# Kernel tuning notes

Hardware: AMD Instinct MI355X
Metric: run time of the kernel (lower is better)

The kernel has to match this reference:

```python
import jax, jax.numpy as jnp
import numpy as np

N, E = 50000, 800000
NODE_DIM, EDGE_DIM, HIDDEN = 128, 32, 128


def setup_inputs() -> dict:
    key = jax.random.key(0)
    ks = jax.random.split(key, 12)
    def lin(k, fan_in, shape):
        bound = 1.0 / np.sqrt(fan_in)
        return jax.random.uniform(k, shape, jnp.float32, -bound, bound)
    return {
        "x": jax.random.normal(ks[0], (N, NODE_DIM), jnp.float32),
        "edge_index": jax.random.randint(ks[1], (2, E), 0, N),
        "edge_attr": jax.random.normal(ks[2], (E, EDGE_DIM), jnp.float32),
        # msg MLP: Linear(node+edge -> hidden), Linear(hidden -> hidden)
        "W1": lin(ks[3], NODE_DIM + EDGE_DIM, (HIDDEN, NODE_DIM + EDGE_DIM)),
        "b1": lin(ks[4], NODE_DIM + EDGE_DIM, (HIDDEN,)),
        "W2": lin(ks[5], HIDDEN, (HIDDEN, HIDDEN)),
        "b2": lin(ks[6], HIDDEN, (HIDDEN,)),
        # GRUCell(input=HIDDEN, hidden=NODE_DIM); gate order r,z,n (torch)
        "W_ih": lin(ks[7], NODE_DIM, (3 * NODE_DIM, HIDDEN)),
        "b_ih": lin(ks[8], NODE_DIM, (3 * NODE_DIM,)),
        "W_hh": lin(ks[9], NODE_DIM, (3 * NODE_DIM, NODE_DIM)),
        "b_hh": lin(ks[10], NODE_DIM, (3 * NODE_DIM,)),
    }


def reference(x, edge_index, edge_attr, W1, b1, W2, b2, W_ih, b_ih, W_hh, b_hh):
    src, dst = edge_index[0], edge_index[1]
    # gather + edge MLP: [E, node+edge] -> [E, hidden]
    m_in = jnp.concatenate([x[src], edge_attr], axis=-1)
    h1 = jax.nn.silu(m_in @ W1.T + b1)
    m = jax.nn.silu(h1 @ W2.T + b2)
    # scatter-add messages per destination node
    agg = jax.ops.segment_sum(m, dst, num_segments=x.shape[0])  # [N, hidden]
    # GRUCell: gates in torch order (r, z, n)
    gi = agg @ W_ih.T + b_ih  # [N, 3*node_dim]
    gh = x @ W_hh.T + b_hh
    i_r, i_z, i_n = jnp.split(gi, 3, axis=-1)
    h_r, h_z, h_n = jnp.split(gh, 3, axis=-1)
    r = jax.nn.sigmoid(i_r + h_r)
    z = jax.nn.sigmoid(i_z + h_z)
    n = jnp.tanh(i_n + r * h_n)
    return (1.0 - z) * n + z * x
```

## Files before the change

kernel.cpp:

```cpp
#include <hip/hip_runtime.h>
#include <hip/hip_bf16.h>
#include <cstdint>

typedef __bf16 bf16x8 __attribute__((ext_vector_type(8)));
typedef __bf16 bf16x4 __attribute__((ext_vector_type(4)));
typedef float  f32x4  __attribute__((ext_vector_type(4)));

#define ND 128
#define HID 128

__device__ __forceinline__ f32x4 mfma_bf16(bf16x8 a, bf16x8 b, f32x4 c) {
  return __builtin_amdgcn_mfma_f32_16x16x32_bf16(a, b, c, 0, 0, 0);
}
__device__ __forceinline__ float fast_sigmoid(float x) {
  return __fdividef(1.f, 1.f + __expf(-x));
}
__device__ __forceinline__ float fast_silu(float x) {
  return __fdividef(x, 1.f + __expf(-x));
}
__device__ __forceinline__ float fast_tanh(float x) {
  float cx = fminf(fmaxf(x, -15.f), 15.f);
  float e = __expf(2.f * cx);
  return __fdividef(e - 1.f, e + 1.f);
}

__global__ void cvt_all(const float* __restrict__ s0, __bf16* __restrict__ d0, int c1,
                        const float* __restrict__ s1, __bf16* __restrict__ d1, int c2,
                        const float* __restrict__ s2, __bf16* __restrict__ d2, int c3,
                        const float* __restrict__ s3, __bf16* __restrict__ d3, int c4,
                        const float* __restrict__ s4, __bf16* __restrict__ d4, int c5) {
  int i = blockIdx.x * blockDim.x + threadIdx.x;
  const float* s; __bf16* d; int j;
  if (i < c1)      { s = s0; d = d0; j = i; }
  else if (i < c2) { s = s1; d = d1; j = i - c1; }
  else if (i < c3) { s = s2; d = d2; j = i - c2; }
  else if (i < c4) { s = s3; d = d3; j = i - c3; }
  else if (i < c5) { s = s4; d = d4; j = i - c4; }
  else return;
  const float4* sp = reinterpret_cast<const float4*>(s) + (size_t)j * 2;
  float4 a = sp[0], b = sp[1];
  bf16x8 v;
  v[0] = (__bf16)a.x; v[1] = (__bf16)a.y; v[2] = (__bf16)a.z; v[3] = (__bf16)a.w;
  v[4] = (__bf16)b.x; v[5] = (__bf16)b.y; v[6] = (__bf16)b.z; v[7] = (__bf16)b.w;
  reinterpret_cast<bf16x8*>(d)[j] = v;
}

__global__ void k_hist(const int* __restrict__ dst, int* __restrict__ counts, int E) {
  int e = blockIdx.x * 256 + threadIdx.x;
  if (e < E) atomicAdd(&counts[dst[e]], 1);
}

__global__ void k_blocksum(const int* __restrict__ counts, int* __restrict__ bsum) {
  __shared__ int sd[256];
  int t = threadIdx.x;
  sd[t] = counts[blockIdx.x * 256 + t];
  __syncthreads();
  for (int d = 128; d > 0; d >>= 1) { if (t < d) sd[t] += sd[t + d]; __syncthreads(); }
  if (!t) bsum[blockIdx.x] = sd[0];
}

__global__ void k_scan_bsum(int* __restrict__ bsum, int nb) {
  __shared__ int sd[256];
  int t = threadIdx.x;
  int v = (t < nb) ? bsum[t] : 0;
  sd[t] = v;
  __syncthreads();
  for (int d = 1; d < 256; d <<= 1) {
    int u = (t >= d) ? sd[t - d] : 0;
    __syncthreads();
    sd[t] += u;
    __syncthreads();
  }
  if (t < nb) bsum[t] = sd[t] - v;
}

__global__ void k_scan_write(const int* __restrict__ counts, const int* __restrict__ bsum,
                             int* __restrict__ offsets, int* __restrict__ cursor) {
  __shared__ int sd[256];
  int t = threadIdx.x, b = blockIdx.x;
  int i = b * 256 + t;
  int c = counts[i];
  sd[t] = c;
  __syncthreads();
  for (int d = 1; d < 256; d <<= 1) {
    int u = (t >= d) ? sd[t - d] : 0;
    __syncthreads();
    sd[t] += u;
    __syncthreads();
  }
  int excl = bsum[b] + sd[t] - c;
  offsets[i] = excl;
  cursor[i]  = excl;
  if (b == (int)gridDim.x - 1 && t == 255) offsets[i + 1] = excl + c;
}

__global__ void k_spos(const int* __restrict__ dst, int* __restrict__ cursor,
                       int* __restrict__ spos, int E) {
  int e = blockIdx.x * 256 + threadIdx.x;
  if (e < E) spos[e] = atomicAdd(&cursor[dst[e]], 1);
}

#define TILE_E 64

template <int SORT>
__global__ __launch_bounds__(512, 6) void edge_mlp(
    const __bf16* __restrict__ xb,
    const int*    __restrict__ ei,
    const float*  __restrict__ ea,
    const __bf16* __restrict__ W1b,
    const float*  __restrict__ b1,
    const __bf16* __restrict__ W2b,
    const float*  __restrict__ b2,
    float*  __restrict__ agg,
    __bf16* __restrict__ mbuf,
    const int* __restrict__ spos,
    int E, int ntiles)
{
  __shared__ __bf16 Als[TILE_E * 192];
  __shared__ __bf16 H1[TILE_E * 128];
  char* AlsB = (char*)Als;
  char* H1B  = (char*)H1;

  const int tid = threadIdx.x;
  const int w  = tid >> 6;
  const int l  = tid & 63;
  const int l4 = l >> 4;
  const int lm = l & 15;
  const int jb = w * 16;

  bf16x8 bw1[5], bw2[4];
  {
    const int jr = jb + lm;
#pragma unroll
    for (int kt = 0; kt < 5; ++kt)
      bw1[kt] = *reinterpret_cast<const bf16x8*>(W1b + (size_t)jr * 160 + kt * 32 + l4 * 8);
#pragma unroll
    for (int kt = 0; kt < 4; ++kt)
      bw2[kt] = *reinterpret_cast<const bf16x8*>(W2b + (size_t)jr * 128 + kt * 32 + l4 * 8);
  }
  float4 b1v = *reinterpret_cast<const float4*>(b1 + jb + l4 * 4);
  float4 b2v = *reinterpret_cast<const float4*>(b2 + jb + l4 * 4);
  const int* srcp = ei;
  const int* dstp = ei + E;

  for (int tile = blockIdx.x; tile < ntiles; tile += gridDim.x) {
    const int e0 = tile * TILE_E;

#pragma unroll
    for (int it = 0; it < 2; ++it) {
      int idx = it * 512 + tid;
      int e = idx >> 4, q = idx & 15;
      int s = srcp[e0 + e];
      bf16x8 v = *reinterpret_cast<const bf16x8*>(xb + (size_t)s * ND + q * 8);
      *reinterpret_cast<bf16x8*>(AlsB + e * 384 + ((q ^ (e & 7)) << 4)) = v;
    }
    {
      int e = tid >> 3, q = tid & 7;
      float4 v = reinterpret_cast<const float4*>(ea)[(size_t)(e0 + e) * 8 + q];
      bf16x4 h;
      h[0] = (__bf16)v.x; h[1] = (__bf16)v.y; h[2] = (__bf16)v.z; h[3] = (__bf16)v.w;
      int chunk = 16 + (q >> 1);
      *reinterpret_cast<bf16x4*>(AlsB + e * 384 + ((chunk ^ (e & 7)) << 4) + ((q & 1) << 3)) = h;
    }
    if (SORT && tid < TILE_E) {
      int sp = spos[e0 + tid];
      *reinterpret_cast<int*>(AlsB + tid * 384 + ((20 ^ (tid & 7)) << 4)) = sp;
    }
    __syncthreads();

#pragma unroll
    for (int et = 0; et < 4; ++et) {
      const int e = et * 16 + lm;
      const int sw = lm & 7;
      f32x4 acc = {0.f, 0.f, 0.f, 0.f};
#pragma unroll
      for (int kt = 0; kt < 5; ++kt) {
        bf16x8 bfrag = *reinterpret_cast<const bf16x8*>(AlsB + e * 384 + (((kt * 4 + l4) ^ sw) << 4));
        acc = mfma_bf16(bw1[kt], bfrag, acc);
      }
      bf16x4 h0;
#pragma unroll
      for (int rr = 0; rr < 4; ++rr)
        h0[rr] = (__bf16)fast_silu(acc[rr] + (&b1v.x)[rr]);
      int c0 = w * 2 + (l4 >> 1);
      int inner = (l4 & 1) << 3;
      *reinterpret_cast<bf16x4*>(H1B + e * 256 + ((c0 ^ sw) << 4) + inner) = h0;
    }
    __syncthreads();

#pragma unroll
    for (int et = 0; et < 4; ++et) {
      const int e = et * 16 + lm;
      const int sw = lm & 7;
      f32x4 acc = {0.f, 0.f, 0.f, 0.f};
#pragma unroll
      for (int kt = 0; kt < 4; ++kt) {
        bf16x8 bfrag = *reinterpret_cast<const bf16x8*>(H1B + e * 256 + (((kt * 4 + l4) ^ sw) << 4));
        acc = mfma_bf16(bw2[kt], bfrag, acc);
      }
      if (SORT) {
        bf16x4 m0;
#pragma unroll
        for (int rr = 0; rr < 4; ++rr)
          m0[rr] = (__bf16)fast_silu(acc[rr] + (&b2v.x)[rr]);
        int sp = *reinterpret_cast<const int*>(AlsB + e * 384 + ((20 ^ sw) << 4));
        *reinterpret_cast<bf16x4*>(mbuf + (size_t)sp * HID + jb + l4 * 4) = m0;
      } else {
        int d = dstp[e0 + e];
#pragma unroll
        for (int rr = 0; rr < 4; ++rr)
          atomicAdd(agg + (size_t)d * HID + jb + l4 * 4 + rr,
                    fast_silu(acc[rr] + (&b2v.x)[rr]));
      }
    }
    __syncthreads();
  }
}

__global__ __launch_bounds__(256) void k_aggregate(
    const __bf16* __restrict__ mbuf, const int* __restrict__ offsets,
    __bf16* __restrict__ aggb, int N)
{
  int node = blockIdx.x * 4 + (threadIdx.x >> 6);
  int l = threadIdx.x & 63;
  if (node >= N) return;
  int lo = offsets[node], hi = offsets[node + 1];
  int cnt = hi - lo;
  float s0 = 0.f, s1 = 0.f;
  const uint32_t* p = reinterpret_cast<const uint32_t*>(mbuf) + (size_t)lo * 64 + l;
  int r = 0;
  for (; r + 4 <= cnt; r += 4) {
    uint32_t u0 = p[0], u1 = p[64], u2 = p[128], u3 = p[192];
    p += 256;
    s0 += __uint_as_float(u0 << 16) + __uint_as_float(u1 << 16)
        + __uint_as_float(u2 << 16) + __uint_as_float(u3 << 16);
    s1 += __uint_as_float(u0 & 0xffff0000u) + __uint_as_float(u1 & 0xffff0000u)
        + __uint_as_float(u2 & 0xffff0000u) + __uint_as_float(u3 & 0xffff0000u);
  }
  for (; r < cnt; ++r) {
    uint32_t u = p[0];
    p += 64;
    s0 += __uint_as_float(u << 16);
    s1 += __uint_as_float(u & 0xffff0000u);
  }
  uint32_t o = (uint32_t)__builtin_bit_cast(unsigned short, (__bf16)s0) |
               ((uint32_t)__builtin_bit_cast(unsigned short, (__bf16)s1) << 16);
  reinterpret_cast<uint32_t*>(aggb)[(size_t)node * 64 + l] = o;
}

__global__ __launch_bounds__(512) void gru2(
    const __bf16* __restrict__ aggb,
    const __bf16* __restrict__ xb,
    const float*  __restrict__ x,
    const __bf16* __restrict__ Wih, const float* __restrict__ bih,
    const __bf16* __restrict__ Whh, const float* __restrict__ bhh,
    float* __restrict__ out, int N)
{
  const int tid = threadIdx.x;
  const int w = tid >> 6, l = tid & 63;
  const int l4 = l >> 4, lm = l & 15;
  const int n0 = blockIdx.x * 64;
  const int jb = w * 16;
  const int jr = jb + lm, jz = jr + 128, jn = jr + 256;

  bf16x8 WiR[4], WhR[4], WiZ[4], WhZ[4], WiN[4], WhN[4];
#pragma unroll
  for (int kt = 0; kt < 4; ++kt) {
    int ko = kt * 32 + l4 * 8;
    WiR[kt] = *reinterpret_cast<const bf16x8*>(Wih + (size_t)jr * ND + ko);
    WhR[kt] = *reinterpret_cast<const bf16x8*>(Whh + (size_t)jr * ND + ko);
    WiZ[kt] = *reinterpret_cast<const bf16x8*>(Wih + (size_t)jz * ND + ko);
    WhZ[kt] = *reinterpret_cast<const bf16x8*>(Whh + (size_t)jz * ND + ko);
    WiN[kt] = *reinterpret_cast<const bf16x8*>(Wih + (size_t)jn * ND + ko);
    WhN[kt] = *reinterpret_cast<const bf16x8*>(Whh + (size_t)jn * ND + ko);
  }
  float4 birv, bizv, binv, bhnv;
  {
    int j0 = jb + l4 * 4;
    float4 a = *reinterpret_cast<const float4*>(bih + j0);
    float4 b = *reinterpret_cast<const float4*>(bhh + j0);
    birv = make_float4(a.x + b.x, a.y + b.y, a.z + b.z, a.w + b.w);
    a = *reinterpret_cast<const float4*>(bih + 128 + j0);
    b = *reinterpret_cast<const float4*>(bhh + 128 + j0);
    bizv = make_float4(a.x + b.x, a.y + b.y, a.z + b.z, a.w + b.w);
    binv = *reinterpret_cast<const float4*>(bih + 256 + j0);
    bhnv = *reinterpret_cast<const float4*>(bhh + 256 + j0);
  }

#pragma unroll
  for (int rt = 0; rt < 4; ++rt) {
    const int node = n0 + rt * 16 + lm;
    const bool ok = node < N;
    bf16x8 aA[4], aX[4];
#pragma unroll
    for (int kt = 0; kt < 4; ++kt) {
      int ko = kt * 32 + l4 * 8;
      bf16x8 z8 = {};
      aA[kt] = ok ? *reinterpret_cast<const bf16x8*>(aggb + (size_t)node * ND + ko) : z8;
      aX[kt] = ok ? *reinterpret_cast<const bf16x8*>(xb + (size_t)node * ND + ko) : z8;
    }
    f32x4 aR = {0.f,0.f,0.f,0.f}, aZ = {0.f,0.f,0.f,0.f};
    f32x4 ai = {0.f,0.f,0.f,0.f}, ah = {0.f,0.f,0.f,0.f};
#pragma unroll
    for (int kt = 0; kt < 4; ++kt) {
      aR = mfma_bf16(WiR[kt], aA[kt], aR);
      aR = mfma_bf16(WhR[kt], aX[kt], aR);
      aZ = mfma_bf16(WiZ[kt], aA[kt], aZ);
      aZ = mfma_bf16(WhZ[kt], aX[kt], aZ);
      ai = mfma_bf16(WiN[kt], aA[kt], ai);
      ah = mfma_bf16(WhN[kt], aX[kt], ah);
    }
    if (ok) {
      float4 xv = *reinterpret_cast<const float4*>(x + (size_t)node * ND + jb + l4 * 4);
      float4 ov;
#pragma unroll
      for (int rr = 0; rr < 4; ++rr) {
        float r = fast_sigmoid(aR[rr] + (&birv.x)[rr]);
        float z = fast_sigmoid(aZ[rr] + (&bizv.x)[rr]);
        float n = fast_tanh(ai[rr] + (&binv.x)[rr] + r * (ah[rr] + (&bhnv.x)[rr]));
        (&ov.x)[rr] = (1.f - z) * n + z * (&xv.x)[rr];
      }
      *reinterpret_cast<float4*>(out + (size_t)node * ND + jb + l4 * 4) = ov;
    }
  }
}

extern "C" void kernel_launch(void* const* d_in, const int* in_sizes, int n_in,
                              void* d_out, int out_size, void* d_ws, size_t ws_size,
                              hipStream_t stream) {
  const float* x   = (const float*)d_in[0];
  const int*   ei  = (const int*)d_in[1];
  const float* ea  = (const float*)d_in[2];
  const float* W1  = (const float*)d_in[3];
  const float* b1  = (const float*)d_in[4];
  const float* W2  = (const float*)d_in[5];
  const float* b2  = (const float*)d_in[6];
  const float* Wih = (const float*)d_in[7];
  const float* bih = (const float*)d_in[8];
  const float* Whh = (const float*)d_in[9];
  const float* bhh = (const float*)d_in[10];
  float* out = (float*)d_out;
  const int N = in_sizes[0] / ND;
  const int E = in_sizes[1] / 2;

  const int nb = (N + 255) / 256;
  const int nC = nb * 256;

  char* ws = (char*)d_ws;
  size_t off = 0;
  auto alloc = [&](size_t bytes) -> void* {
    void* p = ws + off;
    off += (bytes + 255) & ~(size_t)255;
    return p;
  };
  __bf16* xb   = (__bf16*)alloc((size_t)N * ND * 2);
  __bf16* aggb = (__bf16*)alloc((size_t)N * ND * 2);
  __bf16* W1b  = (__bf16*)alloc(128 * 160 * 2);
  __bf16* W2b  = (__bf16*)alloc(128 * 128 * 2);
  __bf16* Wihb = (__bf16*)alloc(384 * 128 * 2);
  __bf16* Whhb = (__bf16*)alloc(384 * 128 * 2);
  size_t common_off = off;

  int*    counts  = (int*)alloc((size_t)nC * 4);
  int*    offsets = (int*)alloc((size_t)(nC + 16) * 4);
  int*    cursor  = (int*)alloc((size_t)nC * 4);
  int*    bsum    = (int*)alloc(256 * 4);
  int*    spos    = (int*)alloc((size_t)E * 4);
  __bf16* mbuf    = (__bf16*)alloc((size_t)E * HID * 2);
  size_t need_sort = off;

  bool use_sort = (ws_size >= need_sort);

  const int n8_x = N * ND / 8, n8_1 = 128 * 160 / 8, n8_2 = 128 * 128 / 8, n8_g = 384 * 128 / 8;
  int c1 = n8_x, c2 = c1 + n8_1, c3 = c2 + n8_2, c4 = c3 + n8_g, c5 = c4 + n8_g;
  cvt_all<<<(c5 + 255) / 256, 256, 0, stream>>>(x, xb, c1, W1, W1b, c2, W2, W2b, c3,
                                                Wih, Wihb, c4, Whh, Whhb, c5);

  const int ntiles = E / TILE_E;
  const int* dstp = ei + E;

  if (use_sort) {
    hipMemsetAsync(counts, 0, (size_t)nC * 4, stream);
    k_hist<<<(E + 255) / 256, 256, 0, stream>>>(dstp, counts, E);
    k_blocksum<<<nb, 256, 0, stream>>>(counts, bsum);
    k_scan_bsum<<<1, 256, 0, stream>>>(bsum, nb);
    k_scan_write<<<nb, 256, 0, stream>>>(counts, bsum, offsets, cursor);
    k_spos<<<(E + 255) / 256, 256, 0, stream>>>(dstp, cursor, spos, E);
    edge_mlp<1><<<2500, 512, 0, stream>>>(xb, ei, ea, W1b, b1, W2b, b2,
                                          nullptr, mbuf, spos, E, ntiles);
    k_aggregate<<<(N + 3) / 4, 256, 0, stream>>>(mbuf, offsets, aggb, N);
  } else {
    off = common_off;
    float* aggf = (float*)alloc((size_t)N * ND * 4);
    hipMemsetAsync(aggf, 0, (size_t)N * ND * 4, stream);
    edge_mlp<0><<<2500, 512, 0, stream>>>(xb, ei, ea, W1b, b1, W2b, b2,
                                          aggf, nullptr, nullptr, E, ntiles);
    cvt_all<<<(n8_x + 255) / 256, 256, 0, stream>>>(aggf, aggb, n8_x,
                                                    nullptr, nullptr, n8_x,
                                                    nullptr, nullptr, n8_x,
                                                    nullptr, nullptr, n8_x,
                                                    nullptr, nullptr, n8_x);
  }

  gru2<<<(N + 63) / 64, 512, 0, stream>>>(aggb, xb, x, Wihb, bih, Whhb, bhh, out, N);
}
```

Baseline: 390.1 us.

## Process edges in dst-sorted order and fuse segmented reduction into edge MLP

Builds a dst-sorted edge permutation and has the edge MLP walk edges in that order. Messages are written to LDS and reduced per destination run inside each tile, with fp32 atomics to agg. This drops the E×128 bf16 message buffer and the separate aggregate kernel, and the kernel also prefetches the next tile's gathers into registers. In exchange, edge_attr and source lookups become indirect gathers, fp32 atomics are still needed, and occupancy is lowered.

New measurement: 365.8 us. 1.07x faster.

```diff
diff --git a/kernel.cpp b/kernel.cpp
--- a/kernel.cpp
+++ b/kernel.cpp
@@ -75,7 +75,7 @@
 }
 
 __global__ void k_scan_write(const int* __restrict__ counts, const int* __restrict__ bsum,
-                             int* __restrict__ offsets, int* __restrict__ cursor) {
+                             int* __restrict__ cursor) {
   __shared__ int sd[256];
   int t = threadIdx.x, b = blockIdx.x;
   int i = b * 256 + t;
@@ -88,38 +88,40 @@
     sd[t] += u;
     __syncthreads();
   }
-  int excl = bsum[b] + sd[t] - c;
-  offsets[i] = excl;
-  cursor[i]  = excl;
-  if (b == (int)gridDim.x - 1 && t == 255) offsets[i + 1] = excl + c;
-}
-
-__global__ void k_spos(const int* __restrict__ dst, int* __restrict__ cursor,
-                       int* __restrict__ spos, int E) {
+  cursor[i] = bsum[b] + sd[t] - c;
+}
+
+__global__ void k_perm(const int* __restrict__ dst, int* __restrict__ cursor,
+                       int* __restrict__ eperm, int* __restrict__ dsorted, int E) {
   int e = blockIdx.x * 256 + threadIdx.x;
-  if (e < E) spos[e] = atomicAdd(&cursor[dst[e]], 1);
+  if (e < E) {
+    int d = dst[e];
+    int p = atomicAdd(&cursor[d], 1);
+    eperm[p] = e;
+    dsorted[p] = d;
+  }
 }
 
 #define TILE_E 64
 
-template <int SORT>
-__global__ __launch_bounds__(512, 6) void edge_mlp(
+__global__ __launch_bounds__(512, 4) void edge_mlp2(
     const __bf16* __restrict__ xb,
-    const int*    __restrict__ ei,
+    const int*    __restrict__ srcp,
     const float*  __restrict__ ea,
     const __bf16* __restrict__ W1b,
     const float*  __restrict__ b1,
     const __bf16* __restrict__ W2b,
     const float*  __restrict__ b2,
-    float*  __restrict__ agg,
-    __bf16* __restrict__ mbuf,
-    const int* __restrict__ spos,
-    int E, int ntiles)
+    const int*    __restrict__ eperm,
+    const int*    __restrict__ dsorted,
+    float* __restrict__ agg,
+    int ntiles)
 {
-  __shared__ __bf16 Als[TILE_E * 192];
+  __shared__ __bf16 Als[TILE_E * 160];
   __shared__ __bf16 H1[TILE_E * 128];
-  char* AlsB = (char*)Als;
-  char* H1B  = (char*)H1;
+  __shared__ int dstls[TILE_E];
+  char* AB = (char*)Als;
+  char* HB = (char*)H1;
 
   const int tid = threadIdx.x;
   const int w  = tid >> 6;
@@ -138,45 +140,72 @@
     for (int kt = 0; kt < 4; ++kt)
       bw2[kt] = *reinterpret_cast<const bf16x8*>(W2b + (size_t)jr * 128 + kt * 32 + l4 * 8);
   }
-  float4 b1v = *reinterpret_cast<const float4*>(b1 + jb + l4 * 4);
-  float4 b2v = *reinterpret_cast<const float4*>(b2 + jb + l4 * 4);
-  const int* srcp = ei;
-  const int* dstp = ei + E;
-
-  for (int tile = blockIdx.x; tile < ntiles; tile += gridDim.x) {
-    const int e0 = tile * TILE_E;
-
-#pragma unroll
-    for (int it = 0; it < 2; ++it) {
-      int idx = it * 512 + tid;
-      int e = idx >> 4, q = idx & 15;
-      int s = srcp[e0 + e];
-      bf16x8 v = *reinterpret_cast<const bf16x8*>(xb + (size_t)s * ND + q * 8);
-      *reinterpret_cast<bf16x8*>(AlsB + e * 384 + ((q ^ (e & 7)) << 4)) = v;
-    }
+  const float4 b1v = *reinterpret_cast<const float4*>(b1 + jb + l4 * 4);
+  const float4 b2v = *reinterpret_cast<const float4*>(b2 + jb + l4 * 4);
+
+  const int fj = tid & 127;
+  const int fg = tid >> 7;
+  const int fchunk = fj >> 3;
+  const int finner = (fj & 7) * 2;
+
+  const int xslot = tid >> 4, xq = tid & 15;
+  const int aslot = tid >> 3, aq = tid & 7;
+
+  bf16x8 pxv0 = {}, pxv1 = {};
+  float4 pea_ = {};
+  int pdst_ = 0;
+
+  auto PREFETCH = [&](int t) {
+    int p0 = t * TILE_E;
+    int e0i = eperm[p0 + xslot];
+    int e1i = eperm[p0 + xslot + 32];
+    int s0 = srcp[e0i];
+    int s1 = srcp[e1i];
+    pxv0 = *reinterpret_cast<const bf16x8*>(xb + (size_t)s0 * ND + xq * 8);
+    pxv1 = *reinterpret_cast<const bf16x8*>(xb + (size_t)s1 * ND + xq * 8);
+    int e2i = eperm[p0 + aslot];
+    pea_ = reinterpret_cast<const float4*>(ea)[(size_t)e2i * 8 + aq];
+    if (tid < TILE_E) pdst_ = dsorted[p0 + tid];
+  };
+
+  int tile = blockIdx.x;
+  if (tile < ntiles) PREFETCH(tile);
+
+  for (; tile < ntiles; tile += gridDim.x) {
+    __syncthreads();
+
     {
-      int e = tid >> 3, q = tid & 7;
-      float4 v = reinterpret_cast<const float4*>(ea)[(size_t)(e0 + e) * 8 + q];
+      int s_ = xslot;
+      *reinterpret_cast<bf16x8*>(AB + s_ * 320 + ((xq ^ (s_ & 7)) << 4)) = pxv0;
+      int s2 = xslot + 32;
+      *reinterpret_cast<bf16x8*>(AB + s2 * 320 + ((xq ^ (s2 & 7)) << 4)) = pxv1;
+    }
+    {
       bf16x4 h;
-      h[0] = (__bf16)v.x; h[1] = (__bf16)v.y; h[2] = (__bf16)v.z; h[3] = (__bf16)v.w;
-      int chunk = 16 + (q >> 1);
-      *reinterpret_cast<bf16x4*>(AlsB + e * 384 + ((chunk ^ (e & 7)) << 4) + ((q & 1) << 3)) = h;
-    }
-    if (SORT && tid < TILE_E) {
-      int sp = spos[e0 + tid];
-      *reinterpret_cast<int*>(AlsB + tid * 384 + ((20 ^ (tid & 7)) << 4)) = sp;
-    }
-    __syncthreads();
+      h[0] = (__bf16)pea_.x; h[1] = (__bf16)pea_.y;
+      h[2] = (__bf16)pea_.z; h[3] = (__bf16)pea_.w;
+      int pc = 16 + ((aq >> 1) ^ (aslot & 3));
+      *reinterpret_cast<bf16x4*>(AB + aslot * 320 + (pc << 4) + ((aq & 1) << 3)) = h;
+    }
+    if (tid < TILE_E) dstls[tid] = pdst_;
+    __syncthreads();
+
+    int nt = tile + gridDim.x;
+    if (nt < ntiles) PREFETCH(nt);
 
 #pragma unroll
     for (int et = 0; et < 4; ++et) {
-      const int e = et * 16 + lm;
-      const int sw = lm & 7;
+      const int s_ = et * 16 + lm;
+      const int sw = s_ & 7;
       f32x4 acc = {0.f, 0.f, 0.f, 0.f};
 #pragma unroll
-      for (int kt = 0; kt < 5; ++kt) {
-        bf16x8 bfrag = *reinterpret_cast<const bf16x8*>(AlsB + e * 384 + (((kt * 4 + l4) ^ sw) << 4));
+      for (int kt = 0; kt < 4; ++kt) {
+        bf16x8 bfrag = *reinterpret_cast<const bf16x8*>(AB + s_ * 320 + (((kt * 4 + l4) ^ sw) << 4));
         acc = mfma_bf16(bw1[kt], bfrag, acc);
+      }
+      {
+        bf16x8 bfrag = *reinterpret_cast<const bf16x8*>(AB + s_ * 320 + ((16 + (l4 ^ (s_ & 3))) << 4));
+        acc = mfma_bf16(bw1[4], bfrag, acc);
       }
       bf16x4 h0;
 #pragma unroll
@@ -184,72 +213,53 @@
         h0[rr] = (__bf16)fast_silu(acc[rr] + (&b1v.x)[rr]);
       int c0 = w * 2 + (l4 >> 1);
       int inner = (l4 & 1) << 3;
-      *reinterpret_cast<bf16x4*>(H1B + e * 256 + ((c0 ^ sw) << 4) + inner) = h0;
+      *reinterpret_cast<bf16x4*>(HB + s_ * 256 + ((c0 ^ sw) << 4) + inner) = h0;
     }
     __syncthreads();
 
 #pragma unroll
     for (int et = 0; et < 4; ++et) {
-      const int e = et * 16 + lm;
-      const int sw = lm & 7;
+      const int s_ = et * 16 + lm;
+      const int sw = s_ & 7;
       f32x4 acc = {0.f, 0.f, 0.f, 0.f};
 #pragma unroll
       for (int kt = 0; kt < 4; ++kt) {
-        bf16x8 bfrag = *reinterpret_cast<const bf16x8*>(H1B + e * 256 + (((kt * 4 + l4) ^ sw) << 4));
+        bf16x8 bfrag = *reinterpret_cast<const bf16x8*>(HB + s_ * 256 + (((kt * 4 + l4) ^ sw) << 4));
         acc = mfma_bf16(bw2[kt], bfrag, acc);
       }
-      if (SORT) {
-        bf16x4 m0;
-#pragma unroll
-        for (int rr = 0; rr < 4; ++rr)
-          m0[rr] = (__bf16)fast_silu(acc[rr] + (&b2v.x)[rr]);
-        int sp = *reinterpret_cast<const int*>(AlsB + e * 384 + ((20 ^ sw) << 4));
-        *reinterpret_cast<bf16x4*>(mbuf + (size_t)sp * HID + jb + l4 * 4) = m0;
-      } else {
-        int d = dstp[e0 + e];
-#pragma unroll
-        for (int rr = 0; rr < 4; ++rr)
-          atomicAdd(agg + (size_t)d * HID + jb + l4 * 4 + rr,
-                    fast_silu(acc[rr] + (&b2v.x)[rr]));
-      }
-    }
-    __syncthreads();
-  }
-}
-
-__global__ __launch_bounds__(256) void k_aggregate(
-    const __bf16* __restrict__ mbuf, const int* __restrict__ offsets,
-    __bf16* __restrict__ aggb, int N)
-{
-  int node = blockIdx.x * 4 + (threadIdx.x >> 6);
-  int l = threadIdx.x & 63;
-  if (node >= N) return;
-  int lo = offsets[node], hi = offsets[node + 1];
-  int cnt = hi - lo;
-  float s0 = 0.f, s1 = 0.f;
-  const uint32_t* p = reinterpret_cast<const uint32_t*>(mbuf) + (size_t)lo * 64 + l;
-  int r = 0;
-  for (; r + 4 <= cnt; r += 4) {
-    uint32_t u0 = p[0], u1 = p[64], u2 = p[128], u3 = p[192];
-    p += 256;
-    s0 += __uint_as_float(u0 << 16) + __uint_as_float(u1 << 16)
-        + __uint_as_float(u2 << 16) + __uint_as_float(u3 << 16);
-    s1 += __uint_as_float(u0 & 0xffff0000u) + __uint_as_float(u1 & 0xffff0000u)
-        + __uint_as_float(u2 & 0xffff0000u) + __uint_as_float(u3 & 0xffff0000u);
-  }
-  for (; r < cnt; ++r) {
-    uint32_t u = p[0];
-    p += 64;
-    s0 += __uint_as_float(u << 16);
-    s1 += __uint_as_float(u & 0xffff0000u);
-  }
-  uint32_t o = (uint32_t)__builtin_bit_cast(unsigned short, (__bf16)s0) |
-               ((uint32_t)__builtin_bit_cast(unsigned short, (__bf16)s1) << 16);
-  reinterpret_cast<uint32_t*>(aggb)[(size_t)node * 64 + l] = o;
+      bf16x4 m0;
+#pragma unroll
+      for (int rr = 0; rr < 4; ++rr)
+        m0[rr] = (__bf16)fast_silu(acc[rr] + (&b2v.x)[rr]);
+      int c0 = w * 2 + (l4 >> 1);
+      int inner = (l4 & 1) << 3;
+      *reinterpret_cast<bf16x4*>(AB + s_ * 256 + ((c0 ^ sw) << 4) + inner) = m0;
+    }
+    __syncthreads();
+
+    {
+      float acc = 0.f;
+      int cur = dstls[fg * 16];
+#pragma unroll
+      for (int i = 0; i < 16; ++i) {
+        int slot = fg * 16 + i;
+        int nd = dstls[slot];
+        if (nd != cur) {
+          atomicAdd(agg + (size_t)cur * HID + fj, acc);
+          acc = 0.f;
+          cur = nd;
+        }
+        uint32_t raw = *reinterpret_cast<const uint16_t*>(
+            AB + slot * 256 + ((fchunk ^ (slot & 7)) << 4) + finner);
+        acc += __uint_as_float(raw << 16);
+      }
+      atomicAdd(agg + (size_t)cur * HID + fj, acc);
+    }
+  }
 }
 
 __global__ __launch_bounds__(512) void gru2(
-    const __bf16* __restrict__ aggb,
+    const float*  __restrict__ agg,
     const __bf16* __restrict__ xb,
     const float*  __restrict__ x,
     const __bf16* __restrict__ Wih, const float* __restrict__ bih,
@@ -296,8 +306,18 @@
     for (int kt = 0; kt < 4; ++kt) {
       int ko = kt * 32 + l4 * 8;
       bf16x8 z8 = {};
-      aA[kt] = ok ? *reinterpret_cast<const bf16x8*>(aggb + (size_t)node * ND + ko) : z8;
-      aX[kt] = ok ? *reinterpret_cast<const bf16x8*>(xb + (size_t)node * ND + ko) : z8;
+      if (ok) {
+        float4 a0 = *reinterpret_cast<const float4*>(agg + (size_t)node * ND + ko);
+        float4 a1 = *reinterpret_cast<const float4*>(agg + (size_t)node * ND + ko + 4);
+        bf16x8 v;
+        v[0] = (__bf16)a0.x; v[1] = (__bf16)a0.y; v[2] = (__bf16)a0.z; v[3] = (__bf16)a0.w;
+        v[4] = (__bf16)a1.x; v[5] = (__bf16)a1.y; v[6] = (__bf16)a1.z; v[7] = (__bf16)a1.w;
+        aA[kt] = v;
+        aX[kt] = *reinterpret_cast<const bf16x8*>(xb + (size_t)node * ND + ko);
+      } else {
+        aA[kt] = z8;
+        aX[kt] = z8;
+      }
     }
     f32x4 aR = {0.f,0.f,0.f,0.f}, aZ = {0.f,0.f,0.f,0.f};
     f32x4 ai = {0.f,0.f,0.f,0.f}, ah = {0.f,0.f,0.f,0.f};
@@ -353,54 +373,39 @@
     off += (bytes + 255) & ~(size_t)255;
     return p;
   };
-  __bf16* xb   = (__bf16*)alloc((size_t)N * ND * 2);
-  __bf16* aggb = (__bf16*)alloc((size_t)N * ND * 2);
-  __bf16* W1b  = (__bf16*)alloc(128 * 160 * 2);
-  __bf16* W2b  = (__bf16*)alloc(128 * 128 * 2);
-  __bf16* Wihb = (__bf16*)alloc(384 * 128 * 2);
-  __bf16* Whhb = (__bf16*)alloc(384 * 128 * 2);
-  size_t common_off = off;
-
+  __bf16* xb      = (__bf16*)alloc((size_t)N * ND * 2);
+  __bf16* W1b     = (__bf16*)alloc(128 * 160 * 2);
+  __bf16* W2b     = (__bf16*)alloc(128 * 128 * 2);
+  __bf16* Wihb    = (__bf16*)alloc(384 * 128 * 2);
+  __bf16* Whhb    = (__bf16*)alloc(384 * 128 * 2);
   int*    counts  = (int*)alloc((size_t)nC * 4);
-  int*    offsets = (int*)alloc((size_t)(nC + 16) * 4);
   int*    cursor  = (int*)alloc((size_t)nC * 4);
   int*    bsum    = (int*)alloc(256 * 4);
-  int*    spos    = (int*)alloc((size_t)E * 4);
-  __bf16* mbuf    = (__bf16*)alloc((size_t)E * HID * 2);
-  size_t need_sort = off;
-
-  bool use_sort = (ws_size >= need_sort);
+  int*    eperm   = (int*)alloc((size_t)E * 4);
+  int*    dsorted = (int*)alloc((size_t)E * 4);
+  float*  agg     = (float*)alloc((size_t)N * ND * 4);
+  (void)ws_size;
+
+  const int* srcp = ei;
+  const int* dstp = ei + E;
+
+  hipMemsetAsync(agg, 0, (size_t)N * ND * 4, stream);
+  hipMemsetAsync(counts, 0, (size_t)nC * 4, stream);
 
   const int n8_x = N * ND / 8, n8_1 = 128 * 160 / 8, n8_2 = 128 * 128 / 8, n8_g = 384 * 128 / 8;
   int c1 = n8_x, c2 = c1 + n8_1, c3 = c2 + n8_2, c4 = c3 + n8_g, c5 = c4 + n8_g;
   cvt_all<<<(c5 + 255) / 256, 256, 0, stream>>>(x, xb, c1, W1, W1b, c2, W2, W2b, c3,
                                                 Wih, Wihb, c4, Whh, Whhb, c5);
 
+  k_hist<<<(E + 255) / 256, 256, 0, stream>>>(dstp, counts, E);
+  k_blocksum<<<nb, 256, 0, stream>>>(counts, bsum);
+  k_scan_bsum<<<1, 256, 0, stream>>>(bsum, nb);
+  k_scan_write<<<nb, 256, 0, stream>>>(counts, bsum, cursor);
+  k_perm<<<(E + 255) / 256, 256, 0, stream>>>(dstp, cursor, eperm, dsorted, E);
+
   const int ntiles = E / TILE_E;
-  const int* dstp = ei + E;
-
-  if (use_sort) {
-    hipMemsetAsync(counts, 0, (size_t)nC * 4, stream);
-    k_hist<<<(E + 255) / 256, 256, 0, stream>>>(dstp, counts, E);
-    k_blocksum<<<nb, 256, 0, stream>>>(counts, bsum);
-    k_scan_bsum<<<1, 256, 0, stream>>>(bsum, nb);
-    k_scan_write<<<nb, 256, 0, stream>>>(counts, bsum, offsets, cursor);
-    k_spos<<<(E + 255) / 256, 256, 0, stream>>>(dstp, cursor, spos, E);
-    edge_mlp<1><<<2500, 512, 0, stream>>>(xb, ei, ea, W1b, b1, W2b, b2,
-                                          nullptr, mbuf, spos, E, ntiles);
-    k_aggregate<<<(N + 3) / 4, 256, 0, stream>>>(mbuf, offsets, aggb, N);
-  } else {
-    off = common_off;
-    float* aggf = (float*)alloc((size_t)N * ND * 4);
-    hipMemsetAsync(aggf, 0, (size_t)N * ND * 4, stream);
-    edge_mlp<0><<<2500, 512, 0, stream>>>(xb, ei, ea, W1b, b1, W2b, b2,
-                                          aggf, nullptr, nullptr, E, ntiles);
-    cvt_all<<<(n8_x + 255) / 256, 256, 0, stream>>>(aggf, aggb, n8_x,
-                                                    nullptr, nullptr, n8_x,
-                                                    nullptr, nullptr, n8_x,
-                                                    nullptr, nullptr, n8_x,
-                                                    nullptr, nullptr, n8_x);
-  }
-
-  gru2<<<(N + 63) / 64, 512, 0, stream>>>(aggb, xb, x, Wihb, bih, Whhb, bhh, out, N);
-}
+  edge_mlp2<<<2500, 512, 0, stream>>>(xb, srcp, ea, W1b, b1, W2b, b2,
+                                      eperm, dsorted, agg, ntiles);
+
+  gru2<<<(N + 63) / 64, 512, 0, stream>>>(agg, xb, x, Wihb, bih, Whhb, bhh, out, N);
+}
```
